# Optimization experiments

Measured on AMD Instinct MI355X. Metric: run time of the kernel, lower is better.

The kernel has to match this reference:

```python
import jax, jax.numpy as jnp
import numpy as np

HEADS = 16
DIM_HEAD = 64
SCALE = DIM_HEAD ** -0.5


def setup_inputs() -> dict:
    key = jax.random.key(0)
    k1, k2, k3 = jax.random.split(key, 3)
    B, N, C = 2, 2048, 1024
    inner = HEADS * DIM_HEAD  # 1024
    x = jax.random.normal(k1, (B, N, C), dtype=jnp.float32)
    w_qkv = jax.random.normal(k2, (C, 3 * inner), dtype=jnp.float32) * (C ** -0.5)
    w_proj = jax.random.normal(k3, (inner, C), dtype=jnp.float32) * (inner ** -0.5)
    b_proj = jnp.zeros((C,), dtype=jnp.float32)
    return {"x": x, "w_qkv": w_qkv, "w_proj": w_proj, "b_proj": b_proj}


def reference(x, w_qkv, w_proj, b_proj):
    B, N, C = x.shape
    qkv = x @ w_qkv  # [B, N, 3*inner]
    qkv = qkv.reshape(B, N, 3, HEADS, DIM_HEAD)
    qkv = jnp.transpose(qkv, (2, 0, 3, 1, 4))  # [3, B, H, N, D]
    q, k, v = qkv[0], qkv[1], qkv[2]
    q = q * SCALE
    attn = jnp.einsum('bhnd,bhmd->bhnm', q, k)  # [B, H, N, N]
    attn = jax.nn.softmax(attn, axis=-1)
    out = jnp.einsum('bhnm,bhmd->bhnd', attn, v)  # [B, H, N, D]
    out = jnp.transpose(out, (0, 2, 1, 3)).reshape(B, N, HEADS * DIM_HEAD)
    return out @ w_proj + b_proj
```

## Files before the change

### kernel.cpp

```cpp
#include <hip/hip_runtime.h>
#include <hip/hip_bf16.h>
#include <cstdint>
#include <cstddef>

static constexpr int BATCH = 2;
static constexpr int SEQ   = 2048;
static constexpr int CDIM  = 1024;
static constexpr int ROWS  = BATCH * SEQ;
static constexpr int QKVN  = 3 * CDIM;
static constexpr int QKN   = 2 * CDIM;

typedef short bf16x8 __attribute__((ext_vector_type(8)));
typedef short bf16x4 __attribute__((ext_vector_type(4)));
typedef float f32x4  __attribute__((ext_vector_type(4)));

__device__ inline short f2bf(float f) {
    union { float f; unsigned u; } v; v.f = f;
    unsigned u = v.u;
    u += 0x7fffu + ((u >> 16) & 1u);
    return (short)(u >> 16);
}

__device__ inline unsigned pk_bf16(float a, float b) {
#if __has_builtin(__builtin_amdgcn_cvt_pk_bf16_f32)
    auto r = __builtin_amdgcn_cvt_pk_bf16_f32(a, b);
    return __builtin_bit_cast(unsigned, r);
#else
    union { float f; unsigned u; } ua, ub;
    ua.f = a; ub.f = b;
    unsigned xa = ua.u + 0x7fffu + ((ua.u >> 16) & 1u);
    unsigned xb = ub.u + 0x7fffu + ((ub.u >> 16) & 1u);
    return __builtin_amdgcn_perm(xb, xa, 0x07060302);
#endif
}

__device__ inline void glds16(const short* g, short* l) {
    __builtin_amdgcn_global_load_lds(
        (const __attribute__((address_space(1))) void*)g,
        (__attribute__((address_space(3))) void*)l, 16, 0, 0);
}

__device__ inline f32x4 mfma16_bf16(bf16x4 a, bf16x4 b, f32x4 c) {
#if __has_builtin(__builtin_amdgcn_mfma_f32_16x16x16bf16_1k)
    return __builtin_amdgcn_mfma_f32_16x16x16bf16_1k(a, b, c, 0, 0, 0);
#else
    asm("v_mfma_f32_16x16x16_bf16 %0, %1, %2, %0" : "+v"(c) : "v"(a), "v"(b));
    return c;
#endif
}

__global__ __launch_bounds__(256) void prep(const float* __restrict__ x,
                                            const float* __restrict__ wqkv,
                                            const float* __restrict__ wproj,
                                            short* __restrict__ x_bf,
                                            short* __restrict__ wqkvT,
                                            short* __restrict__ wprojT,
                                            float smul) {
    __shared__ float tile[32][33];
    const int bid = blockIdx.x, t = threadIdx.x;
    if (bid < 4096) {
        int i = bid * 256 + t;
        float4 f = ((const float4*)x)[i];
        uint2 o;
        o.x = pk_bf16(f.x, f.y);
        o.y = pk_bf16(f.z, f.w);
        ((uint2*)x_bf)[i] = o;
        return;
    }
    const float* in; short* out; int C, r0, c0; float scale; int srows;
    if (bid < 7168) {
        int b2 = bid - 4096;
        in = wqkv; out = wqkvT; C = QKVN;
        c0 = (b2 % 96) * 32; r0 = (b2 / 96) * 32;
        scale = smul; srows = 1024;
    } else {
        int b3 = bid - 7168;
        in = wproj; out = wprojT; C = CDIM;
        c0 = (b3 & 31) * 32; r0 = (b3 >> 5) * 32;
        scale = 1.0f; srows = 0;
    }
    int tx = t & 31, ty = t >> 5;
    #pragma unroll
    for (int i = 0; i < 4; i++)
        tile[ty + i * 8][tx] = in[(size_t)(r0 + ty + i * 8) * C + c0 + tx];
    __syncthreads();
    #pragma unroll
    for (int i = 0; i < 4; i++) {
        int orow = c0 + ty + i * 8;
        float sc = (orow < srows) ? scale : 1.0f;
        out[(size_t)orow * CDIM + r0 + tx] = f2bf(tile[tx][ty + i * 8] * sc);
    }
}

template<int BF16OUT, int MT>
__device__ __forceinline__ void gemm_core(const short* __restrict__ A,
                                          const short* __restrict__ Bt,
                                          void* __restrict__ C,
                                          const float* __restrict__ bias,
                                          int N, int K, int m0, int n0,
                                          short* As, short* Bs) {
    constexpr int AF = MT / 32;
    const int t = threadIdx.x, wave = t >> 6, lane = t & 63;
    const int l15 = lane & 15, quad = lane >> 4;
    const int wr = wave >> 1, wc = wave & 1;

    f32x4 acc[AF][4] = {};

    const short* gA = A  + (size_t)(m0 + wave * (MT / 4) + (lane >> 2)) * K + (lane & 3) * 8;
    const short* gB = Bt + (size_t)(n0 + wave * 32 + (lane >> 2)) * K + (lane & 3) * 8;
    short* lA = &As[wave * (MT / 4) * 32];
    short* lB = &Bs[wave * 32 * 32];

    for (int k0 = 0; k0 < K; k0 += 32) {
        glds16(gA + k0, lA);
        if constexpr (MT == 128) glds16(gA + 16 * K + k0, lA + 512);
        glds16(gB + k0,          lB);
        glds16(gB + 16 * K + k0, lB + 512);
        __syncthreads();

        bf16x8 af[AF], bf[4];
        #pragma unroll
        for (int i = 0; i < AF; i++)
            af[i] = *(const bf16x8*)&As[(wr * (MT / 2) + i * 16 + l15) * 32 + quad * 8];
        #pragma unroll
        for (int j = 0; j < 4; j++)
            bf[j] = *(const bf16x8*)&Bs[(wc * 64 + j * 16 + l15) * 32 + quad * 8];
        #pragma unroll
        for (int i = 0; i < AF; i++)
            #pragma unroll
            for (int j = 0; j < 4; j++)
                acc[i][j] = __builtin_amdgcn_mfma_f32_16x16x32_bf16(af[i], bf[j], acc[i][j], 0, 0, 0);
        __syncthreads();
    }

    #pragma unroll
    for (int i = 0; i < AF; i++) {
        #pragma unroll
        for (int j = 0; j < 4; j++) {
            #pragma unroll
            for (int r = 0; r < 4; r++) {
                int row = m0 + wr * (MT / 2) + i * 16 + quad * 4 + r;
                int col = n0 + wc * 64 + j * 16 + l15;
                float v = acc[i][j][r];
                if (BF16OUT) ((short*)C)[(size_t)row * N + col] = f2bf(v);
                else         ((float*)C)[(size_t)row * N + col] = v + bias[col];
            }
        }
    }
}

__global__ __launch_bounds__(256) void gemm_qk_v(const short* __restrict__ x_bf,
                                                 const short* __restrict__ wqkvT,
                                                 short* __restrict__ qk,
                                                 short* __restrict__ vT) {
    __shared__ __align__(16) short As[128 * 32];
    __shared__ __align__(16) short Bs[128 * 32];
    const int bid = blockIdx.x;
    if (bid < 512) {
        gemm_core<1, 128>(x_bf, wqkvT, qk, nullptr, QKN, CDIM,
                          (bid >> 4) * 128, (bid & 15) * 128, As, Bs);
    } else {
        int b2 = bid - 512;
        gemm_core<1, 64>(wqkvT + (size_t)QKN * CDIM, x_bf, vT, nullptr, ROWS, CDIM,
                         (b2 >> 5) * 64, (b2 & 31) * 128, As, Bs);
    }
}

__global__ __launch_bounds__(256) void gemm_proj(const short* __restrict__ A,
                                                 const short* __restrict__ Bt,
                                                 float* __restrict__ C,
                                                 const float* __restrict__ bias) {
    __shared__ __align__(16) short As[64 * 32];
    __shared__ __align__(16) short Bs[128 * 32];
    gemm_core<0, 64>(A, Bt, C, bias, CDIM, CDIM,
                     blockIdx.y * 64, blockIdx.x * 128, As, Bs);
}

static constexpr int KBUF  = 2 * 128 * 32;
static constexpr int VOFF  = 2 * KBUF;
static constexpr int LDV   = 136;
static constexpr int VBUF  = 64 * LDV;
static constexpr int SMEM_SH = VOFF + 2 * VBUF;

__global__ __launch_bounds__(512) void attn_kernel(const short* __restrict__ qk,
                                                   const short* __restrict__ vTg,
                                                   short* __restrict__ attn_out) {
    __shared__ __align__(16) short smem[SMEM_SH];

    const int t = threadIdx.x, wave = t >> 6, lane = t & 63;
    const int l15 = lane & 15, quad = lane >> 4;
    const int bh = blockIdx.y, b = bh >> 4, h = bh & 15;
    const int q0 = blockIdx.x * 128;
    const size_t baseQ = (size_t)(b * SEQ) * QKN + h * 64;

    const size_t qoff = baseQ + (size_t)(q0 + wave * 16 + l15) * QKN + quad * 8;
    bf16x8 qf0 = *(const bf16x8*)&qk[qoff];
    bf16x8 qf1 = *(const bf16x8*)&qk[qoff + 32];

    const short* gK = qk + baseQ + 1024
                    + (size_t)(wave * 16 + (lane >> 2)) * QKN + (lane & 3) * 8;
    const short* gV = vTg + (size_t)(h * 64) * ROWS + b * SEQ;
    const int vd = t >> 3, vc = t & 7;

    const bf16x4 ones = { (short)0x3F80, (short)0x3F80, (short)0x3F80, (short)0x3F80 };

    f32x4 ot[4] = {};
    f32x4 ol = {};

    glds16(gK,      smem + wave * 512);
    glds16(gK + 32, smem + 4096 + wave * 512);
    {
        int4 va = *(const int4*)&gV[(size_t)vd * ROWS + vc * 8];
        int4 vb = *(const int4*)&gV[(size_t)vd * ROWS + 64 + vc * 8];
        *(int4*)&smem[VOFF + vd * LDV + vc * 8]      = va;
        *(int4*)&smem[VOFF + vd * LDV + 64 + vc * 8] = vb;
    }

    for (int j = 0; j < SEQ / 128; j++) {
        const int cur = j & 1, nxt = cur ^ 1;
        __syncthreads();

        int4 va, vb;
        if (j < SEQ / 128 - 1) {
            const size_t jadd = (size_t)(j + 1) * 128 * QKN;
            glds16(gK + jadd,      smem + nxt * KBUF + wave * 512);
            glds16(gK + jadd + 32, smem + nxt * KBUF + 4096 + wave * 512);
            va = *(const int4*)&gV[(size_t)vd * ROWS + (j + 1) * 128 + vc * 8];
            vb = *(const int4*)&gV[(size_t)vd * ROWS + (j + 1) * 128 + 64 + vc * 8];
        }

        const short* Kb0 = smem + cur * KBUF;
        const short* Kb1 = Kb0 + 4096;
        const short* Vb  = smem + VOFF + cur * VBUF;

        #pragma unroll
        for (int sub = 0; sub < 8; sub++) {
            bf16x8 kf0 = *(const bf16x8*)&Kb0[(sub * 16 + l15) * 32 + quad * 8];
            bf16x8 kf1 = *(const bf16x8*)&Kb1[(sub * 16 + l15) * 32 + quad * 8];
            f32x4 a = {};
            a = __builtin_amdgcn_mfma_f32_16x16x32_bf16(kf0, qf0, a, 0, 0, 0);
            a = __builtin_amdgcn_mfma_f32_16x16x32_bf16(kf1, qf1, a, 0, 0, 0);
            float p0 = __builtin_amdgcn_exp2f(a[0]);
            float p1 = __builtin_amdgcn_exp2f(a[1]);
            float p2 = __builtin_amdgcn_exp2f(a[2]);
            float p3 = __builtin_amdgcn_exp2f(a[3]);
            union { unsigned u[2]; bf16x4 v; } pu;
            pu.u[0] = pk_bf16(p0, p1);
            pu.u[1] = pk_bf16(p2, p3);
            ol = mfma16_bf16(ones, pu.v, ol);
            #pragma unroll
            for (int d = 0; d < 4; d++) {
                bf16x4 vf = *(const bf16x4*)&Vb[(d * 16 + l15) * LDV + sub * 16 + quad * 4];
                ot[d] = mfma16_bf16(vf, pu.v, ot[d]);
            }
        }

        if (j < SEQ / 128 - 1) {
            *(int4*)&smem[VOFF + nxt * VBUF + vd * LDV + vc * 8]      = va;
            *(int4*)&smem[VOFF + nxt * VBUF + vd * LDV + 64 + vc * 8] = vb;
        }
    }

    float inv = 1.0f / ol[0];
    #pragma unroll
    for (int d = 0; d < 4; d++) {
        unsigned w0 = pk_bf16(ot[d][0] * inv, ot[d][1] * inv);
        unsigned w1 = pk_bf16(ot[d][2] * inv, ot[d][3] * inv);
        *(unsigned*)&smem[(wave * 16 + l15) * 72 + d * 16 + quad * 4]     = w0;
        *(unsigned*)&smem[(wave * 16 + l15) * 72 + d * 16 + quad * 4 + 2] = w1;
    }
    __syncthreads();
    {
        int row = t >> 3, ch = t & 7;
        #pragma unroll
        for (int p = 0; p < 2; p++) {
            int rr = row + p * 64;
            int4 v = *(const int4*)&smem[rr * 72 + ch * 8];
            *(int4*)&attn_out[(size_t)(b * SEQ + q0 + rr) * CDIM + h * 64 + ch * 8] = v;
        }
    }
}

extern "C" void kernel_launch(void* const* d_in, const int* in_sizes, int n_in,
                              void* d_out, int out_size, void* d_ws, size_t ws_size,
                              hipStream_t stream) {
    const float* x      = (const float*)d_in[0];
    const float* w_qkv  = (const float*)d_in[1];
    const float* w_proj = (const float*)d_in[2];
    const float* b_proj = (const float*)d_in[3];
    float* out = (float*)d_out;

    char* ws = (char*)d_ws;
    short* x_bf    = (short*)(ws);
    short* wqkvT   = (short*)(ws + 8388608);
    short* wprojT  = (short*)(ws + 14680064);
    short* qk_bf   = (short*)(ws + 16777216);
    short* vTg     = (short*)(ws + 33554432);
    short* attn_bf = (short*)(ws + 41943040);

    const float SMUL = 0.125f * 1.44269504088896340736f;

    prep<<<8192, 256, 0, stream>>>(x, w_qkv, w_proj, x_bf, wqkvT, wprojT, SMUL);

    gemm_qk_v<<<1024, 256, 0, stream>>>(x_bf, wqkvT, qk_bf, vTg);

    attn_kernel<<<dim3(SEQ / 128, BATCH * 16), 512, 0, stream>>>(qk_bf, vTg, attn_bf);

    gemm_proj<<<dim3(CDIM / 128, ROWS / 64), 256, 0, stream>>>(attn_bf, wprojT, out, b_proj);
}
```

Baseline: 200.9 us.

## Process two 16-row query tiles per wave in attention, halving block threads

The attention kernel now runs 4 waves per block instead of 8, and each wave handles 32 query rows as two 16-row tiles. Each K and V fragment read from shared memory is reused by both tiles, which halves LDS reads per MFMA. Loads of K and V are redistributed over the smaller thread count, and a barrier is added before the output staging. The cost is more accumulator registers per thread and fewer waves per block to hide latency.

```diff
diff --git a/kernel.cpp b/kernel.cpp
--- a/kernel.cpp
+++ b/kernel.cpp
@@ -182,7 +182,7 @@
 static constexpr int VBUF  = 64 * LDV;
 static constexpr int SMEM_SH = VOFF + 2 * VBUF;
 
-__global__ __launch_bounds__(512) void attn_kernel(const short* __restrict__ qk,
+__global__ __launch_bounds__(256) void attn_kernel(const short* __restrict__ qk,
                                                    const short* __restrict__ vTg,
                                                    short* __restrict__ attn_out) {
     __shared__ __align__(16) short smem[SMEM_SH];
@@ -193,40 +193,48 @@
     const int q0 = blockIdx.x * 128;
     const size_t baseQ = (size_t)(b * SEQ) * QKN + h * 64;
 
-    const size_t qoff = baseQ + (size_t)(q0 + wave * 16 + l15) * QKN + quad * 8;
-    bf16x8 qf0 = *(const bf16x8*)&qk[qoff];
-    bf16x8 qf1 = *(const bf16x8*)&qk[qoff + 32];
+    const size_t qoff0 = baseQ + (size_t)(q0 + wave * 32 + l15) * QKN + quad * 8;
+    const size_t qoff1 = qoff0 + (size_t)16 * QKN;
+    bf16x8 qf00 = *(const bf16x8*)&qk[qoff0];
+    bf16x8 qf01 = *(const bf16x8*)&qk[qoff0 + 32];
+    bf16x8 qf10 = *(const bf16x8*)&qk[qoff1];
+    bf16x8 qf11 = *(const bf16x8*)&qk[qoff1 + 32];
 
     const short* gK = qk + baseQ + 1024
-                    + (size_t)(wave * 16 + (lane >> 2)) * QKN + (lane & 3) * 8;
+                    + (size_t)(wave * 32 + (lane >> 2)) * QKN + (lane & 3) * 8;
     const short* gV = vTg + (size_t)(h * 64) * ROWS + b * SEQ;
-    const int vd = t >> 3, vc = t & 7;
+    const int vd = t >> 2, vc = t & 3;
 
     const bf16x4 ones = { (short)0x3F80, (short)0x3F80, (short)0x3F80, (short)0x3F80 };
 
-    f32x4 ot[4] = {};
-    f32x4 ol = {};
-
-    glds16(gK,      smem + wave * 512);
-    glds16(gK + 32, smem + 4096 + wave * 512);
-    {
-        int4 va = *(const int4*)&gV[(size_t)vd * ROWS + vc * 8];
-        int4 vb = *(const int4*)&gV[(size_t)vd * ROWS + 64 + vc * 8];
-        *(int4*)&smem[VOFF + vd * LDV + vc * 8]      = va;
-        *(int4*)&smem[VOFF + vd * LDV + 64 + vc * 8] = vb;
+    f32x4 ot0[4] = {}, ot1[4] = {};
+    f32x4 ol0 = {}, ol1 = {};
+
+    glds16(gK,                 smem + wave * 1024);
+    glds16(gK + 16 * QKN,      smem + wave * 1024 + 512);
+    glds16(gK + 32,            smem + 4096 + wave * 1024);
+    glds16(gK + 16 * QKN + 32, smem + 4096 + wave * 1024 + 512);
+    #pragma unroll
+    for (int c = 0; c < 4; c++) {
+        int4 v = *(const int4*)&gV[(size_t)vd * ROWS + vc * 8 + c * 32];
+        *(int4*)&smem[VOFF + vd * LDV + vc * 8 + c * 32] = v;
     }
 
     for (int j = 0; j < SEQ / 128; j++) {
         const int cur = j & 1, nxt = cur ^ 1;
         __syncthreads();
 
-        int4 va, vb;
+        int4 va[4];
         if (j < SEQ / 128 - 1) {
             const size_t jadd = (size_t)(j + 1) * 128 * QKN;
-            glds16(gK + jadd,      smem + nxt * KBUF + wave * 512);
-            glds16(gK + jadd + 32, smem + nxt * KBUF + 4096 + wave * 512);
-            va = *(const int4*)&gV[(size_t)vd * ROWS + (j + 1) * 128 + vc * 8];
-            vb = *(const int4*)&gV[(size_t)vd * ROWS + (j + 1) * 128 + 64 + vc * 8];
+            short* kb = smem + nxt * KBUF + wave * 1024;
+            glds16(gK + jadd,                 kb);
+            glds16(gK + jadd + 16 * QKN,      kb + 512);
+            glds16(gK + jadd + 32,            kb + 4096);
+            glds16(gK + jadd + 16 * QKN + 32, kb + 4096 + 512);
+            #pragma unroll
+            for (int c = 0; c < 4; c++)
+                va[c] = *(const int4*)&gV[(size_t)vd * ROWS + (j + 1) * 128 + vc * 8 + c * 32];
         }
 
         const short* Kb0 = smem + cur * KBUF;
@@ -237,46 +245,52 @@
         for (int sub = 0; sub < 8; sub++) {
             bf16x8 kf0 = *(const bf16x8*)&Kb0[(sub * 16 + l15) * 32 + quad * 8];
             bf16x8 kf1 = *(const bf16x8*)&Kb1[(sub * 16 + l15) * 32 + quad * 8];
-            f32x4 a = {};
-            a = __builtin_amdgcn_mfma_f32_16x16x32_bf16(kf0, qf0, a, 0, 0, 0);
-            a = __builtin_amdgcn_mfma_f32_16x16x32_bf16(kf1, qf1, a, 0, 0, 0);
-            float p0 = __builtin_amdgcn_exp2f(a[0]);
-            float p1 = __builtin_amdgcn_exp2f(a[1]);
-            float p2 = __builtin_amdgcn_exp2f(a[2]);
-            float p3 = __builtin_amdgcn_exp2f(a[3]);
-            union { unsigned u[2]; bf16x4 v; } pu;
-            pu.u[0] = pk_bf16(p0, p1);
-            pu.u[1] = pk_bf16(p2, p3);
-            ol = mfma16_bf16(ones, pu.v, ol);
+            f32x4 a0 = {}, a1 = {};
+            a0 = __builtin_amdgcn_mfma_f32_16x16x32_bf16(kf0, qf00, a0, 0, 0, 0);
+            a0 = __builtin_amdgcn_mfma_f32_16x16x32_bf16(kf1, qf01, a0, 0, 0, 0);
+            a1 = __builtin_amdgcn_mfma_f32_16x16x32_bf16(kf0, qf10, a1, 0, 0, 0);
+            a1 = __builtin_amdgcn_mfma_f32_16x16x32_bf16(kf1, qf11, a1, 0, 0, 0);
+            union { unsigned u[2]; bf16x4 v; } pu0, pu1;
+            pu0.u[0] = pk_bf16(__builtin_amdgcn_exp2f(a0[0]), __builtin_amdgcn_exp2f(a0[1]));
+            pu0.u[1] = pk_bf16(__builtin_amdgcn_exp2f(a0[2]), __builtin_amdgcn_exp2f(a0[3]));
+            pu1.u[0] = pk_bf16(__builtin_amdgcn_exp2f(a1[0]), __builtin_amdgcn_exp2f(a1[1]));
+            pu1.u[1] = pk_bf16(__builtin_amdgcn_exp2f(a1[2]), __builtin_amdgcn_exp2f(a1[3]));
+            ol0 = mfma16_bf16(ones, pu0.v, ol0);
+            ol1 = mfma16_bf16(ones, pu1.v, ol1);
             #pragma unroll
             for (int d = 0; d < 4; d++) {
                 bf16x4 vf = *(const bf16x4*)&Vb[(d * 16 + l15) * LDV + sub * 16 + quad * 4];
-                ot[d] = mfma16_bf16(vf, pu.v, ot[d]);
+                ot0[d] = mfma16_bf16(vf, pu0.v, ot0[d]);
+                ot1[d] = mfma16_bf16(vf, pu1.v, ot1[d]);
             }
         }
 
         if (j < SEQ / 128 - 1) {
-            *(int4*)&smem[VOFF + nxt * VBUF + vd * LDV + vc * 8]      = va;
-            *(int4*)&smem[VOFF + nxt * VBUF + vd * LDV + 64 + vc * 8] = vb;
-        }
-    }
-
-    float inv = 1.0f / ol[0];
+            #pragma unroll
+            for (int c = 0; c < 4; c++)
+                *(int4*)&smem[VOFF + nxt * VBUF + vd * LDV + vc * 8 + c * 32] = va[c];
+        }
+    }
+
+    __syncthreads();
+    float inv0 = 1.0f / ol0[0], inv1 = 1.0f / ol1[0];
     #pragma unroll
     for (int d = 0; d < 4; d++) {
-        unsigned w0 = pk_bf16(ot[d][0] * inv, ot[d][1] * inv);
-        unsigned w1 = pk_bf16(ot[d][2] * inv, ot[d][3] * inv);
-        *(unsigned*)&smem[(wave * 16 + l15) * 72 + d * 16 + quad * 4]     = w0;
-        *(unsigned*)&smem[(wave * 16 + l15) * 72 + d * 16 + quad * 4 + 2] = w1;
+        int r0 = (wave * 32 + l15) * 72 + d * 16 + quad * 4;
+        *(unsigned*)&smem[r0]     = pk_bf16(ot0[d][0] * inv0, ot0[d][1] * inv0);
+        *(unsigned*)&smem[r0 + 2] = pk_bf16(ot0[d][2] * inv0, ot0[d][3] * inv0);
+        int r1 = (wave * 32 + 16 + l15) * 72 + d * 16 + quad * 4;
+        *(unsigned*)&smem[r1]     = pk_bf16(ot1[d][0] * inv1, ot1[d][1] * inv1);
+        *(unsigned*)&smem[r1 + 2] = pk_bf16(ot1[d][2] * inv1, ot1[d][3] * inv1);
     }
     __syncthreads();
     {
-        int row = t >> 3, ch = t & 7;
-        #pragma unroll
-        for (int p = 0; p < 2; p++) {
-            int rr = row + p * 64;
-            int4 v = *(const int4*)&smem[rr * 72 + ch * 8];
-            *(int4*)&attn_out[(size_t)(b * SEQ + q0 + rr) * CDIM + h * 64 + ch * 8] = v;
+        int row = t >> 1, c2 = t & 1;
+        #pragma unroll
+        for (int p = 0; p < 4; p++) {
+            int ch = c2 * 4 + p;
+            int4 v = *(const int4*)&smem[row * 72 + ch * 8];
+            *(int4*)&attn_out[(size_t)(b * SEQ + q0 + row) * CDIM + h * 64 + ch * 8] = v;
         }
     }
 }
@@ -304,7 +318,7 @@
 
     gemm_qk_v<<<1024, 256, 0, stream>>>(x_bf, wqkvT, qk_bf, vTg);
 
-    attn_kernel<<<dim3(SEQ / 128, BATCH * 16), 512, 0, stream>>>(qk_bf, vTg, attn_bf);
+    attn_kernel<<<dim3(SEQ / 128, BATCH * 16), 256, 0, stream>>>(qk_bf, vTg, attn_bf);
 
     gemm_proj<<<dim3(CDIM / 128, ROWS / 64), 256, 0, stream>>>(attn_bf, wprojT, out, b_proj);
 }
```

Result: slower. 211.7 us (+5.4%).
